# Kernel optimization log

Measured on AMD Instinct MI355X. Metric: run time of the kernel, lower is better.

The kernel has to match this reference:

```python
import jax, jax.numpy as jnp
import numpy as np

K_AMP = 6.0 ** 0.5      # self.k = sqrt(6) amplification
RES_SCALE = 0.1
EPS_NORM = 5e-05        # F.normalize eps
EPS_KERN = 1e-4         # performer softmax_kernel eps


def setup_inputs() -> dict:
    key = jax.random.key(0)
    ks = jax.random.split(key, 6)
    N, C, H, W = 16, 128, 128, 128
    Cr = C // 2            # reduction=2 -> dim_heads=64
    M = 128                # nb_features
    s = (1.0 / C) ** 0.5   # fan-in scaling for 1x1 conv weights
    return {
        "x": jax.random.normal(ks[0], (N, C, H, W), jnp.float32),
        "w1": jax.random.normal(ks[1], (Cr, C), jnp.float32) * s,
        "b1": jnp.zeros((Cr,), jnp.float32),
        "w2": jax.random.normal(ks[2], (Cr, C), jnp.float32) * s,
        "b2": jnp.zeros((Cr,), jnp.float32),
        "wa": jax.random.normal(ks[3], (C, C), jnp.float32) * s,
        "ba": jnp.zeros((C,), jnp.float32),
        "proj": jax.random.normal(ks[4], (M, Cr), jnp.float32),  # random-feature projection (buffer)
    }


def _l2norm(t):
    n = jnp.linalg.norm(t, axis=-1, keepdims=True)
    return t / jnp.maximum(n, EPS_NORM)


def reference(x, w1, b1, w2, b2, wa, ba, proj):
    N, C, H, W = x.shape
    xt = x.transpose(0, 2, 3, 1).reshape(N, H * W, C)   # [N, HW, C] tokens
    # 1x1 convs == per-token linears
    q = _l2norm(xt @ w1.T + b1) * K_AMP                 # [N, HW, Cr]
    k = _l2norm(xt @ w2.T + b2) * K_AMP                 # [N, HW, Cr]
    v = xt @ wa.T + ba                                  # [N, HW, C]
    # Performer FAVOR+ softmax-kernel feature maps
    d = q.shape[-1]
    dn = d ** -0.25                                     # data normalizer d^(-1/4)
    ratio = proj.shape[0] ** -0.5                       # m^(-1/2)
    qd = jnp.einsum('nid,md->nim', q * dn, proj)        # [N, HW, M]
    kd = jnp.einsum('nid,md->nim', k * dn, proj)
    q_diag = jnp.sum(q * q, axis=-1, keepdims=True) * 0.5 * dn * dn
    k_diag = jnp.sum(k * k, axis=-1, keepdims=True) * 0.5 * dn * dn
    qp = ratio * (jnp.exp(qd - q_diag - jnp.max(qd, axis=-1, keepdims=True)) + EPS_KERN)
    kp = ratio * (jnp.exp(kd - k_diag - jnp.max(kd)) + EPS_KERN)   # global max for keys
    # linear attention: out = (qp @ (kp^T v)) / (qp @ sum(kp))
    ksum = jnp.sum(kp, axis=1)                          # [N, M]
    d_inv = 1.0 / jnp.einsum('nim,nm->ni', qp, ksum)    # [N, HW]
    ctx = jnp.einsum('nim,nie->nme', kp, v)             # [N, M, C]
    out = jnp.einsum('nme,nim,ni->nie', ctx, qp, d_inv) # [N, HW, C]
    return out.transpose(0, 2, 1).reshape(N, C, H, W) * RES_SCALE
```

## Files before the change

kernel.cpp:

```cpp
#include <hip/hip_runtime.h>
#include <hip/hip_bf16.h>
#include <cstdio>
#include <cstdint>

#define HWD 16384
#define NB  16
#define CD  128
#define CR  64
#define MF  128

constexpr float K_AMP = 2.4494897427831781f;
constexpr float DN    = 0.35355339059327379f;
constexpr float RATIO = 0.088388347648318447f;
constexpr float EPSN  = 5e-5f;
constexpr float EPSK  = 1e-4f;
constexpr float RES   = 0.1f;
constexpr float DIAG  = 0.375f;

typedef __attribute__((ext_vector_type(4))) float f32x4;
typedef __attribute__((ext_vector_type(8))) short s16x8;

__device__ __forceinline__ short f2bf(float f) {
  __hip_bfloat16 h = __float2bfloat16(f);
  short s; __builtin_memcpy(&s, &h, 2); return s;
}
__device__ __forceinline__ float bf2f_s(short s) {
  __hip_bfloat16 h; __builtin_memcpy(&h, &s, 2); return __bfloat162float(h);
}
__device__ __forceinline__ f32x4 mfma16(s16x8 a, s16x8 b, f32x4 c) {
  return __builtin_amdgcn_mfma_f32_16x16x32_bf16(a, b, c, 0, 0, 0);
}

constexpr size_t OFF_QP   = 0;
constexpr size_t OFF_EP   = OFF_QP   + 16777216;
constexpr size_t OFF_GP   = OFF_EP   + 16777216;
constexpr size_t OFF_G    = OFF_GP   + 8388608;
constexpr size_t OFF_CTXB = OFF_G    + 262144;
constexpr size_t OFF_KSUM = OFF_CTXB + 131072;
constexpr size_t OFF_XSUM = OFF_KSUM + 2048;
constexpr size_t OFF_KSUMB= OFF_XSUM + 2048;
constexpr size_t OFF_XSUMB= OFF_KSUMB+ 262144;
constexpr size_t OFF_BMAX = OFF_XSUMB+ 262144;
constexpr size_t OFF_SBLK = OFF_BMAX + 2048;
constexpr size_t OFF_W1B  = OFF_SBLK + 2048;
constexpr size_t OFF_W2B  = OFF_W1B  + 4096;
constexpr size_t OFF_PB   = OFF_W2B  + 4096;
constexpr size_t WS_FLOATS = OFF_PB  + 4096;

__global__ void k_prep(const float* __restrict__ w1, const float* __restrict__ w2,
                       const float* __restrict__ proj,
                       short* __restrict__ w1b, short* __restrict__ w2b, short* __restrict__ pb) {
  int t = blockIdx.x * 256 + threadIdx.x;
  w1b[t] = f2bf(w1[t]);
  w2b[t] = f2bf(w2[t]);
  pb[t]  = f2bf(proj[t]);
}

__device__ __forceinline__ void qk_gemms(const short* __restrict__ wb,
                                         const float* __restrict__ bsh,
                                         const short* __restrict__ pb,
                                         const short* Xt, short* Qt,
                                         int tid, f32x4 (&acc2)[8][2]) {
  const int lane = tid & 63, w = tid >> 6;
  const int l15 = lane & 15, q4 = lane >> 4;
  f32x4 acc1[4][2];
  #pragma unroll
  for (int ct = 0; ct < 4; ct++)
    #pragma unroll
    for (int it = 0; it < 2; it++) acc1[ct][it] = {0.f, 0.f, 0.f, 0.f};
  #pragma unroll
  for (int ks = 0; ks < 4; ks++) {
    s16x8 bfr[2];
    #pragma unroll
    for (int it = 0; it < 2; it++)
      bfr[it] = *(const s16x8*)&Xt[(w * 32 + it * 16 + l15) * 136 + ks * 32 + q4 * 8];
    #pragma unroll
    for (int ct = 0; ct < 4; ct++) {
      s16x8 afr = *(const s16x8*)&wb[(ct * 16 + l15) * 128 + ks * 32 + q4 * 8];
      #pragma unroll
      for (int it = 0; it < 2; it++) acc1[ct][it] = mfma16(afr, bfr[it], acc1[ct][it]);
    }
  }
  float qv[4][2][4];
  float ss[2] = {0.f, 0.f};
  #pragma unroll
  for (int ct = 0; ct < 4; ct++)
    #pragma unroll
    for (int it = 0; it < 2; it++)
      #pragma unroll
      for (int r = 0; r < 4; r++) {
        float v = acc1[ct][it][r] + bsh[ct * 16 + q4 * 4 + r];
        qv[ct][it][r] = v;
        ss[it] = fmaf(v, v, ss[it]);
      }
  #pragma unroll
  for (int it = 0; it < 2; it++) {
    ss[it] += __shfl_xor(ss[it], 16);
    ss[it] += __shfl_xor(ss[it], 32);
  }
  float scale[2];
  #pragma unroll
  for (int it = 0; it < 2; it++)
    scale[it] = (K_AMP * DN) / fmaxf(sqrtf(ss[it]), EPSN);
  __syncthreads();
  #pragma unroll
  for (int it = 0; it < 2; it++)
    #pragma unroll
    for (int ct = 0; ct < 4; ct++) {
      short4 pk;
      pk.x = f2bf(qv[ct][it][0] * scale[it]);
      pk.y = f2bf(qv[ct][it][1] * scale[it]);
      pk.z = f2bf(qv[ct][it][2] * scale[it]);
      pk.w = f2bf(qv[ct][it][3] * scale[it]);
      *(short4*)&Qt[(w * 32 + it * 16 + l15) * 72 + ct * 16 + q4 * 4] = pk;
    }
  __syncthreads();
  #pragma unroll
  for (int mt = 0; mt < 8; mt++)
    #pragma unroll
    for (int it = 0; it < 2; it++) acc2[mt][it] = {0.f, 0.f, 0.f, 0.f};
  #pragma unroll
  for (int ks = 0; ks < 2; ks++) {
    s16x8 afr[2];
    #pragma unroll
    for (int it = 0; it < 2; it++)
      afr[it] = *(const s16x8*)&Qt[(w * 32 + it * 16 + l15) * 72 + ks * 32 + q4 * 8];
    #pragma unroll
    for (int mt = 0; mt < 8; mt++) {
      s16x8 bfr = *(const s16x8*)&pb[(mt * 16 + l15) * 64 + ks * 32 + q4 * 8];
      #pragma unroll
      for (int it = 0; it < 2; it++) acc2[mt][it] = mfma16(afr[it], bfr, acc2[mt][it]);
    }
  }
}

__global__ __launch_bounds__(256) void k_qkf(
    const float* __restrict__ x,
    const short* __restrict__ w1b, const float* __restrict__ b1,
    const short* __restrict__ w2b, const float* __restrict__ b2,
    const short* __restrict__ pb,
    short* __restrict__ qp, short* __restrict__ ep,
    float* __restrict__ bmax, float* __restrict__ ksumb, float* __restrict__ xsumb) {
  const int n = blockIdx.y, i0 = blockIdx.x * 128;
  const int tid = threadIdx.x, lane = tid & 63, w = tid >> 6;
  const int l15 = lane & 15, q4 = lane >> 4;
  __shared__ __align__(16) short Xt[128 * 136];
  __shared__ __align__(16) char smemQ[128 * 72 * 2];
  __shared__ float bsh[128];
  __shared__ float wred[4];
  short* Qt = (short*)smemQ;
  float* sred = (float*)smemQ;
  if (tid < 64) bsh[tid] = b1[tid];
  else if (tid < 128) bsh[tid] = b2[tid - 64];
  #pragma unroll
  for (int u = 0; u < 16; u++) {
    int id = u * 256 + tid;
    int i = id & 127, cg = id >> 7;
    const float* xp = x + ((size_t)(n * CD + cg * 4) * HWD + i0 + i);
    short4 pk;
    pk.x = f2bf(xp[0]); pk.y = f2bf(xp[HWD]);
    pk.z = f2bf(xp[2 * HWD]); pk.w = f2bf(xp[3 * HWD]);
    *(short4*)&Xt[i * 136 + cg * 4] = pk;
  }
  __syncthreads();

  f32x4 acc2[8][2];

  qk_gemms(w1b, bsh, pb, Xt, Qt, tid, acc2);
  #pragma unroll
  for (int it = 0; it < 2; it++)
    #pragma unroll
    for (int r = 0; r < 4; r++) {
      float mx = -3.0e38f;
      #pragma unroll
      for (int mt = 0; mt < 8; mt++) mx = fmaxf(mx, acc2[mt][it][r]);
      mx = fmaxf(mx, __shfl_xor(mx, 1));
      mx = fmaxf(mx, __shfl_xor(mx, 2));
      mx = fmaxf(mx, __shfl_xor(mx, 4));
      mx = fmaxf(mx, __shfl_xor(mx, 8));
      int i = i0 + w * 32 + it * 16 + q4 * 4 + r;
      #pragma unroll
      for (int mt = 0; mt < 8; mt++) {
        float e = RATIO * (__expf(acc2[mt][it][r] - DIAG - mx) + EPSK);
        qp[((size_t)n * HWD + i) * MF + mt * 16 + l15] = f2bf(e);
      }
    }

  qk_gemms(w2b, bsh + 64, pb, Xt, Qt, tid, acc2);
  float mxk = -3.0e38f;
  #pragma unroll
  for (int mt = 0; mt < 8; mt++)
    #pragma unroll
    for (int it = 0; it < 2; it++)
      #pragma unroll
      for (int r = 0; r < 4; r++) mxk = fmaxf(mxk, acc2[mt][it][r]);
  #pragma unroll
  for (int d = 1; d < 64; d <<= 1) mxk = fmaxf(mxk, __shfl_xor(mxk, d));
  if (lane == 0) wred[w] = mxk;
  __syncthreads();
  const float bm = fmaxf(fmaxf(wred[0], wred[1]), fmaxf(wred[2], wred[3]));
  float es[8];
  #pragma unroll
  for (int mt = 0; mt < 8; mt++) es[mt] = 0.f;
  #pragma unroll
  for (int it = 0; it < 2; it++)
    #pragma unroll
    for (int r = 0; r < 4; r++) {
      int i = i0 + w * 32 + it * 16 + q4 * 4 + r;
      #pragma unroll
      for (int mt = 0; mt < 8; mt++) {
        float e = __expf(acc2[mt][it][r] - bm);
        es[mt] += e;
        ep[((size_t)n * HWD + i) * MF + mt * 16 + l15] = f2bf(e);
      }
    }
  #pragma unroll
  for (int mt = 0; mt < 8; mt++) {
    es[mt] += __shfl_xor(es[mt], 16);
    es[mt] += __shfl_xor(es[mt], 32);
  }
  if (q4 == 0) {
    #pragma unroll
    for (int mt = 0; mt < 8; mt++) sred[w * 128 + mt * 16 + l15] = es[mt];
  }
  {
    int c = tid & 127, half = tid >> 7;
    float xs = 0.f;
    #pragma unroll 16
    for (int u = 0; u < 64; u++) xs += bf2f_s(Xt[(half * 64 + u) * 136 + c]);
    sred[512 + tid] = xs;
  }
  __syncthreads();
  const size_t pb0 = ((size_t)n * 128 + blockIdx.x) * 128;
  if (tid < 128) {
    ksumb[pb0 + tid] = sred[tid] + sred[128 + tid] + sred[256 + tid] + sred[384 + tid];
  } else {
    int c = tid - 128;
    xsumb[pb0 + c] = sred[512 + c] + sred[640 + c];
  }
  if (tid == 0) bmax[n * 128 + blockIdx.x] = bm;
}

__global__ void k_ksum(const float* __restrict__ bmax, const float* __restrict__ ksumb,
                       const float* __restrict__ xsumb, float* __restrict__ sblk,
                       float* __restrict__ ksum, float* __restrict__ xsum) {
  __shared__ float red[256];
  __shared__ float sb_sh[256];
  int t = threadIdx.x;
  float v = -3.0e38f;
  #pragma unroll
  for (int u = 0; u < 8; u++) v = fmaxf(v, bmax[t + 256 * u]);
  red[t] = v;
  __syncthreads();
  for (int s = 128; s > 0; s >>= 1) {
    if (t < s) red[t] = fmaxf(red[t], red[t + s]);
    __syncthreads();
  }
  const float gm = red[0];
  int g = blockIdx.x * 256 + t;
  int n = g >> 7, m = g & 127;
  float sv = RATIO * __expf(bmax[g] - gm - DIAG);
  sb_sh[t] = sv;
  sblk[g] = sv;
  __syncthreads();
  const float* kb = ksumb + ((size_t)n << 14) + m;
  const float* xb = xsumb + ((size_t)n << 14) + m;
  const float* sb = &sb_sh[(t >> 7) * 128];
  float s = 0.f, xs = 0.f;
  #pragma unroll 4
  for (int b = 0; b < 128; b++) {
    s = fmaf(sb[b], kb[(size_t)b * 128], s);
    xs += xb[(size_t)b * 128];
  }
  ksum[g] = s + RATIO * EPSK * 16384.0f;
  xsum[g] = xs;
}

__global__ __launch_bounds__(256) void k_g(const float* __restrict__ x,
                                           const short* __restrict__ ep,
                                           const float* __restrict__ sblk,
                                           float* __restrict__ gp) {
  const int slab = blockIdx.x, n = blockIdx.y;
  const int t = threadIdx.x, lane = t & 63, w = t >> 6;
  const int l15 = lane & 15, q4 = lane >> 4;
  __shared__ short kl[64 * 136];
  __shared__ short xl[128 * 72];
  f32x4 acc[2][8];
  #pragma unroll
  for (int mt = 0; mt < 2; mt++)
    #pragma unroll
    for (int ct = 0; ct < 8; ct++) acc[mt][ct] = {0.f, 0.f, 0.f, 0.f};
  for (int ch = 0; ch < 8; ch++) {
    int ib = slab * 512 + ch * 64;
    const float sf = sblk[n * 128 + slab * 4 + (ch >> 1)];
    __syncthreads();
    #pragma unroll
    for (int u = 0; u < 4; u++) {
      int id = u * 256 + t, ii = id >> 4, m8 = (id & 15) * 8;
      *(s16x8*)&kl[ii * 136 + m8] =
          *(const s16x8*)&ep[((size_t)n * HWD + ib + ii) * MF + m8];
    }
    #pragma unroll
    for (int u = 0; u < 8; u++) {
      int id = u * 256 + t, c = id >> 4, i4 = (id & 15) * 4;
      const float4 v = *(const float4*)(x + ((size_t)n * CD + c) * HWD + ib + i4);
      short4 pk;
      pk.x = f2bf(v.x * sf); pk.y = f2bf(v.y * sf);
      pk.z = f2bf(v.z * sf); pk.w = f2bf(v.w * sf);
      *(short4*)&xl[c * 72 + i4] = pk;
    }
    __syncthreads();
    #pragma unroll
    for (int ks = 0; ks < 2; ks++) {
      s16x8 afr[2];
      #pragma unroll
      for (int mt = 0; mt < 2; mt++) {
        int m = w * 32 + mt * 16 + l15;
        short tmp[8];
        #pragma unroll
        for (int j = 0; j < 8; j++) tmp[j] = kl[(ks * 32 + q4 * 8 + j) * 136 + m];
        afr[mt] = *(s16x8*)tmp;
      }
      #pragma unroll
      for (int ct = 0; ct < 8; ct++) {
        s16x8 bfr = *(const s16x8*)&xl[(ct * 16 + l15) * 72 + ks * 32 + q4 * 8];
        #pragma unroll
        for (int mt = 0; mt < 2; mt++) acc[mt][ct] = mfma16(afr[mt], bfr, acc[mt][ct]);
      }
    }
  }
  float* g = gp + (((size_t)slab * NB + n) << 14);
  #pragma unroll
  for (int mt = 0; mt < 2; mt++)
    #pragma unroll
    for (int ct = 0; ct < 8; ct++)
      #pragma unroll
      for (int r = 0; r < 4; r++)
        g[(w * 32 + mt * 16 + q4 * 4 + r) * CD + ct * 16 + l15] = acc[mt][ct][r];
}

__global__ void k_gred(const float* __restrict__ gp, const float* __restrict__ xsum,
                       float* __restrict__ G) {
  int t = blockIdx.x * 256 + threadIdx.x;
  int n = t >> 14, r = t & 16383;
  float s = 0.f;
  #pragma unroll
  for (int sc = 0; sc < 32; sc++) s += gp[(((size_t)sc * NB + n) << 14) + r];
  G[((size_t)n << 14) + r] = s + (RATIO * EPSK) * xsum[n * 128 + (r & 127)];
}

__global__ __launch_bounds__(256) void k_ctx(const float* __restrict__ G,
                                             const float* __restrict__ wa,
                                             const float* __restrict__ ba,
                                             const float* __restrict__ ksum,
                                             short* __restrict__ ctxb) {
  int n = blockIdx.x;
  int tm = threadIdx.x & 15, tc = threadIdx.x >> 4;
  const float* Gn = G + ((size_t)n << 14);
  float acc[8][8];
  #pragma unroll
  for (int a = 0; a < 8; a++)
    #pragma unroll
    for (int b = 0; b < 8; b++) acc[a][b] = 0.f;
  for (int c2 = 0; c2 < CD; c2 += 4) {
    float4 g4[8], w4[8];
    #pragma unroll
    for (int a = 0; a < 8; a++) g4[a] = *(const float4*)&Gn[(tm * 8 + a) * CD + c2];
    #pragma unroll
    for (int b = 0; b < 8; b++) w4[b] = *(const float4*)&wa[(tc * 8 + b) * CD + c2];
    #pragma unroll
    for (int a = 0; a < 8; a++)
      #pragma unroll
      for (int b = 0; b < 8; b++) {
        acc[a][b] = fmaf(g4[a].x, w4[b].x, acc[a][b]);
        acc[a][b] = fmaf(g4[a].y, w4[b].y, acc[a][b]);
        acc[a][b] = fmaf(g4[a].z, w4[b].z, acc[a][b]);
        acc[a][b] = fmaf(g4[a].w, w4[b].w, acc[a][b]);
      }
  }
  #pragma unroll
  for (int a = 0; a < 8; a++) {
    int m = tm * 8 + a;
    float km = ksum[n * MF + m];
    #pragma unroll
    for (int b = 0; b < 8; b++) {
      int c = tc * 8 + b;
      ctxb[((size_t)n * CD + c) * MF + m] = f2bf(acc[a][b] + ba[c] * km);
    }
  }
}

__global__ __launch_bounds__(256) void k_out(const short* __restrict__ qp,
                                             const short* __restrict__ ctxb,
                                             const float* __restrict__ ksum,
                                             float* __restrict__ out) {
  const int n = blockIdx.y, i0 = blockIdx.x * 128;
  const int t = threadIdx.x, lane = t & 63, w = t >> 6;
  const int l15 = lane & 15, q4 = lane >> 4;
  __shared__ short qt[128 * 136];
  __shared__ float ksl[128];
  __shared__ float dinv[128];
  if (t < 128) ksl[t] = ksum[n * MF + t];
  #pragma unroll
  for (int u = 0; u < 8; u++) {
    int id = u * 256 + t, i = id >> 4, m8 = (id & 15) * 8;
    *(s16x8*)&qt[i * 136 + m8] =
        *(const s16x8*)&qp[((size_t)n * HWD + i0 + i) * MF + m8];
  }
  __syncthreads();
  if (t < 128) {
    float s = 0.f;
    #pragma unroll
    for (int mb = 0; mb < 16; mb++) {
      s16x8 v = *(const s16x8*)&qt[t * 136 + mb * 8];
      #pragma unroll
      for (int j = 0; j < 8; j++) s = fmaf(bf2f_s(v[j]), ksl[mb * 8 + j], s);
    }
    dinv[t] = RES / s;
  }
  f32x4 acc[8][2];
  #pragma unroll
  for (int it = 0; it < 8; it++)
    #pragma unroll
    for (int ct = 0; ct < 2; ct++) acc[it][ct] = {0.f, 0.f, 0.f, 0.f};
  #pragma unroll
  for (int ks = 0; ks < 4; ks++) {
    s16x8 afr[2];
    #pragma unroll
    for (int ct = 0; ct < 2; ct++)
      afr[ct] = *(const s16x8*)&ctxb[((size_t)n * CD + w * 32 + ct * 16 + l15) * MF +
                                     ks * 32 + q4 * 8];
    #pragma unroll
    for (int it = 0; it < 8; it++) {
      s16x8 bfr = *(const s16x8*)&qt[(it * 16 + l15) * 136 + ks * 32 + q4 * 8];
      #pragma unroll
      for (int ct = 0; ct < 2; ct++) acc[it][ct] = mfma16(afr[ct], bfr, acc[it][ct]);
    }
  }
  __syncthreads();
  #pragma unroll
  for (int it = 0; it < 8; it++) {
    float dv = dinv[it * 16 + l15];
    #pragma unroll
    for (int ct = 0; ct < 2; ct++)
      #pragma unroll
      for (int r = 0; r < 4; r++)
        out[((size_t)n * CD + w * 32 + ct * 16 + q4 * 4 + r) * HWD + i0 + it * 16 + l15] =
            acc[it][ct][r] * dv;
  }
}

extern "C" void kernel_launch(void* const* d_in, const int* in_sizes, int n_in,
                              void* d_out, int out_size, void* d_ws, size_t ws_size,
                              hipStream_t stream) {
  (void)in_sizes; (void)n_in; (void)out_size;
  const float* x    = (const float*)d_in[0];
  const float* w1   = (const float*)d_in[1];
  const float* b1   = (const float*)d_in[2];
  const float* w2   = (const float*)d_in[3];
  const float* b2   = (const float*)d_in[4];
  const float* wa   = (const float*)d_in[5];
  const float* ba   = (const float*)d_in[6];
  const float* proj = (const float*)d_in[7];
  float* ws  = (float*)d_ws;
  float* out = (float*)d_out;

  if (ws_size < WS_FLOATS * sizeof(float)) {
    fprintf(stderr, "ENLCA: workspace too small: need %zu, have %zu\n",
            WS_FLOATS * sizeof(float), ws_size);
  }

  short* qpB   = (short*)(ws + OFF_QP);
  short* epB   = (short*)(ws + OFF_EP);
  float* gpF   = ws + OFF_GP;
  float* GF    = ws + OFF_G;
  short* ctxB  = (short*)(ws + OFF_CTXB);
  float* ksumF = ws + OFF_KSUM;
  float* xsumF = ws + OFF_XSUM;
  float* ksumbF= ws + OFF_KSUMB;
  float* xsumbF= ws + OFF_XSUMB;
  float* bmaxF = ws + OFF_BMAX;
  float* sblkF = ws + OFF_SBLK;
  short* w1B   = (short*)(ws + OFF_W1B);
  short* w2B   = (short*)(ws + OFF_W2B);
  short* pB    = (short*)(ws + OFF_PB);

  k_prep<<<32, 256, 0, stream>>>(w1, w2, proj, w1B, w2B, pB);
  k_qkf<<<dim3(128, 16), 256, 0, stream>>>(x, w1B, b1, w2B, b2, pB,
                                           qpB, epB, bmaxF, ksumbF, xsumbF);
  k_ksum<<<8, 256, 0, stream>>>(bmaxF, ksumbF, xsumbF, sblkF, ksumF, xsumF);
  k_g<<<dim3(32, 16), 256, 0, stream>>>(x, epB, sblkF, gpF);
  k_gred<<<1024, 256, 0, stream>>>(gpF, xsumF, GF);
  k_ctx<<<16, 256, 0, stream>>>(GF, wa, ba, ksumF, ctxB);
  k_out<<<dim3(128, 16), 256, 0, stream>>>(qpB, ctxB, ksumF, out);
}
```

Baseline: 466.8 us.

## Spread ctx GEMM over more blocks and shrink qkf shared memory

The k_ctx kernel previously launched only 16 blocks, each computing an 8x8 register tile. It now launches 128 blocks where each thread computes 8 outputs for one feature row, trading register reuse for far more parallelism across CUs. In k_qkf the Q staging buffer loses its padding (stride 72 to 64), and the partial-sum scratch that aliased it is replaced by small shared arrays accumulated with shared-memory atomics, reducing LDS footprint. The unpadded stride may introduce LDS bank conflicts, and the atomics make the float summation order nondeterministic.

Measured after the change: 443.1 us. -5.1%, faster.

```diff
diff --git a/kernel.cpp b/kernel.cpp
--- a/kernel.cpp
+++ b/kernel.cpp
@@ -112,7 +112,7 @@
       pk.y = f2bf(qv[ct][it][1] * scale[it]);
       pk.z = f2bf(qv[ct][it][2] * scale[it]);
       pk.w = f2bf(qv[ct][it][3] * scale[it]);
-      *(short4*)&Qt[(w * 32 + it * 16 + l15) * 72 + ct * 16 + q4 * 4] = pk;
+      *(short4*)&Qt[(w * 32 + it * 16 + l15) * 64 + ct * 16 + q4 * 4] = pk;
     }
   __syncthreads();
   #pragma unroll
@@ -124,7 +124,7 @@
     s16x8 afr[2];
     #pragma unroll
     for (int it = 0; it < 2; it++)
-      afr[it] = *(const s16x8*)&Qt[(w * 32 + it * 16 + l15) * 72 + ks * 32 + q4 * 8];
+      afr[it] = *(const s16x8*)&Qt[(w * 32 + it * 16 + l15) * 64 + ks * 32 + q4 * 8];
     #pragma unroll
     for (int mt = 0; mt < 8; mt++) {
       s16x8 bfr = *(const s16x8*)&pb[(mt * 16 + l15) * 64 + ks * 32 + q4 * 8];
@@ -145,13 +145,14 @@
   const int tid = threadIdx.x, lane = tid & 63, w = tid >> 6;
   const int l15 = lane & 15, q4 = lane >> 4;
   __shared__ __align__(16) short Xt[128 * 136];
-  __shared__ __align__(16) char smemQ[128 * 72 * 2];
+  __shared__ __align__(16) short Qt[128 * 64];
   __shared__ float bsh[128];
   __shared__ float wred[4];
-  short* Qt = (short*)smemQ;
-  float* sred = (float*)smemQ;
+  __shared__ float esum[128];
+  __shared__ float xsred[128];
   if (tid < 64) bsh[tid] = b1[tid];
   else if (tid < 128) bsh[tid] = b2[tid - 64];
+  if (tid < 128) { esum[tid] = 0.f; xsred[tid] = 0.f; }
   #pragma unroll
   for (int u = 0; u < 16; u++) {
     int id = u * 256 + tid;
@@ -221,22 +222,22 @@
   }
   if (q4 == 0) {
     #pragma unroll
-    for (int mt = 0; mt < 8; mt++) sred[w * 128 + mt * 16 + l15] = es[mt];
+    for (int mt = 0; mt < 8; mt++) atomicAdd(&esum[mt * 16 + l15], es[mt]);
   }
   {
     int c = tid & 127, half = tid >> 7;
     float xs = 0.f;
     #pragma unroll 16
     for (int u = 0; u < 64; u++) xs += bf2f_s(Xt[(half * 64 + u) * 136 + c]);
-    sred[512 + tid] = xs;
+    atomicAdd(&xsred[c], xs);
   }
   __syncthreads();
   const size_t pb0 = ((size_t)n * 128 + blockIdx.x) * 128;
   if (tid < 128) {
-    ksumb[pb0 + tid] = sred[tid] + sred[128 + tid] + sred[256 + tid] + sred[384 + tid];
+    ksumb[pb0 + tid] = esum[tid];
   } else {
     int c = tid - 128;
-    xsumb[pb0 + c] = sred[512 + c] + sred[640 + c];
+    xsumb[pb0 + c] = xsred[c];
   }
   if (tid == 0) bmax[n * 128 + blockIdx.x] = bm;
 }
@@ -354,39 +355,29 @@
                                              const float* __restrict__ ba,
                                              const float* __restrict__ ksum,
                                              short* __restrict__ ctxb) {
-  int n = blockIdx.x;
-  int tm = threadIdx.x & 15, tc = threadIdx.x >> 4;
+  int n = blockIdx.x >> 3;
+  int m = (blockIdx.x & 7) * 16 + (threadIdx.x & 15);
+  int tc = threadIdx.x >> 4;
   const float* Gn = G + ((size_t)n << 14);
-  float acc[8][8];
-  #pragma unroll
-  for (int a = 0; a < 8; a++)
-    #pragma unroll
-    for (int b = 0; b < 8; b++) acc[a][b] = 0.f;
+  float acc[8];
+  #pragma unroll
+  for (int b = 0; b < 8; b++) acc[b] = 0.f;
   for (int c2 = 0; c2 < CD; c2 += 4) {
-    float4 g4[8], w4[8];
-    #pragma unroll
-    for (int a = 0; a < 8; a++) g4[a] = *(const float4*)&Gn[(tm * 8 + a) * CD + c2];
-    #pragma unroll
-    for (int b = 0; b < 8; b++) w4[b] = *(const float4*)&wa[(tc * 8 + b) * CD + c2];
-    #pragma unroll
-    for (int a = 0; a < 8; a++)
-      #pragma unroll
-      for (int b = 0; b < 8; b++) {
-        acc[a][b] = fmaf(g4[a].x, w4[b].x, acc[a][b]);
-        acc[a][b] = fmaf(g4[a].y, w4[b].y, acc[a][b]);
-        acc[a][b] = fmaf(g4[a].z, w4[b].z, acc[a][b]);
-        acc[a][b] = fmaf(g4[a].w, w4[b].w, acc[a][b]);
-      }
-  }
-  #pragma unroll
-  for (int a = 0; a < 8; a++) {
-    int m = tm * 8 + a;
-    float km = ksum[n * MF + m];
+    float4 g4 = *(const float4*)&Gn[m * CD + c2];
     #pragma unroll
     for (int b = 0; b < 8; b++) {
-      int c = tc * 8 + b;
-      ctxb[((size_t)n * CD + c) * MF + m] = f2bf(acc[a][b] + ba[c] * km);
-    }
+      float4 w4 = *(const float4*)&wa[(tc * 8 + b) * CD + c2];
+      acc[b] = fmaf(g4.x, w4.x, acc[b]);
+      acc[b] = fmaf(g4.y, w4.y, acc[b]);
+      acc[b] = fmaf(g4.z, w4.z, acc[b]);
+      acc[b] = fmaf(g4.w, w4.w, acc[b]);
+    }
+  }
+  float km = ksum[n * MF + m];
+  #pragma unroll
+  for (int b = 0; b < 8; b++) {
+    int c = tc * 8 + b;
+    ctxb[((size_t)n * CD + c) * MF + m] = f2bf(acc[b] + ba[c] * km);
   }
 }
 
@@ -491,6 +482,6 @@
   k_ksum<<<8, 256, 0, stream>>>(bmaxF, ksumbF, xsumbF, sblkF, ksumF, xsumF);
   k_g<<<dim3(32, 16), 256, 0, stream>>>(x, epB, sblkF, gpF);
   k_gred<<<1024, 256, 0, stream>>>(gpF, xsumF, GF);
-  k_ctx<<<16, 256, 0, stream>>>(GF, wa, ba, ksumF, ctxB);
+  k_ctx<<<128, 256, 0, stream>>>(GF, wa, ba, ksumF, ctxB);
   k_out<<<dim3(128, 16), 256, 0, stream>>>(qpB, ctxB, ksumF, out);
 }
```
